# Kernel tuning notes

Hardware: AMD Instinct MI355X
Metric: run time of the kernel (lower is better)

The kernel has to match this reference:

```python
import jax, jax.numpy as jnp
import numpy as np

D_MODEL = 1024
N_HEAD = 16
D_HEAD = D_MODEL // N_HEAD


def setup_inputs() -> dict:
    key = jax.random.key(0)
    k_x, k_wqkv, k_bqkv, k_wp, k_bp = jax.random.split(key, 5)
    B, T = 2, 2048
    bound = 1.0 / np.sqrt(D_MODEL)
    return {
        "x": jax.random.normal(k_x, (B, T, D_MODEL), dtype=jnp.float32),
        "w_qkv": jax.random.uniform(k_wqkv, (D_MODEL, 3 * D_MODEL), jnp.float32, -bound, bound),
        "b_qkv": jax.random.uniform(k_bqkv, (3 * D_MODEL,), jnp.float32, -bound, bound),
        "w_proj": jax.random.uniform(k_wp, (D_MODEL, D_MODEL), jnp.float32, -bound, bound),
        "b_proj": jax.random.uniform(k_bp, (D_MODEL,), jnp.float32, -bound, bound),
    }


def reference(x, w_qkv, b_qkv, w_proj, b_proj):
    B, T, C = x.shape
    qkv = x @ w_qkv + b_qkv                       # [B,T,3C]
    qkv = qkv.reshape(B, T, 3, N_HEAD, D_HEAD)
    qkv = jnp.transpose(qkv, (2, 0, 3, 1, 4))      # [3,B,H,T,dh]
    q, k, v = qkv[0], qkv[1], qkv[2]
    scale = np.sqrt(D_HEAD).astype(np.float32)
    attn = jnp.einsum("bhqd,bhkd->bhqk", q, k) / scale  # [B,H,T,T]
    causal = jnp.tril(jnp.ones((T, T), dtype=bool))
    attn = jnp.where(causal, attn, -jnp.inf)
    attn = jax.nn.softmax(attn, axis=-1)
    out = jnp.einsum("bhqk,bhkd->bhqd", attn, v)   # [B,H,T,dh]
    out = jnp.transpose(out, (0, 2, 1, 3)).reshape(B, T, C)
    return out @ w_proj + b_proj
```

## Files before the change

kernel.cpp:

```cpp
#include <hip/hip_runtime.h>
#include <hip/hip_bf16.h>
#include <math.h>

constexpr int Bb   = 2;
constexpr int T    = 2048;
constexpr int C    = 1024;
constexpr int H    = 16;
constexpr int M    = Bb * T;
constexpr int NQKV = 3 * C;

typedef __attribute__((ext_vector_type(8))) short bf16x8;
typedef __attribute__((ext_vector_type(4))) float f32x4;

__device__ inline short f2bf(float f) {
    __hip_bfloat16 h = __float2bfloat16(f);
    return *reinterpret_cast<short*>(&h);
}

#define GLOBAL_AS __attribute__((address_space(1)))
#define LDS_AS    __attribute__((address_space(3)))

__device__ __forceinline__ void gload_lds16(const short* g, short* s) {
    __builtin_amdgcn_global_load_lds((const GLOBAL_AS void*)g, (LDS_AS void*)s, 16, 0, 0);
}

__global__ __launch_bounds__(256)
void prep_all(const float* __restrict__ x, short* __restrict__ xb,
              const float* __restrict__ w_qkv, short* __restrict__ wqkvt,
              const float* __restrict__ w_proj, short* __restrict__ wprojt)
{
    __shared__ float tile[32][33];
    const int blk = blockIdx.x;
    const int tid = threadIdx.x;

    if (blk < 4096) {
        const int i = blk * 1024 + tid * 4;
        const float4 v = *(const float4*)(x + i);
        short4 s;
        s.x = f2bf(v.x); s.y = f2bf(v.y); s.z = f2bf(v.z); s.w = f2bf(v.w);
        *(short4*)(xb + i) = s;
        return;
    }

    const bool isqkv = (blk < 7168);
    const int bidx = isqkv ? (blk - 4096) : (blk - 7168);
    const int nblk = isqkv ? 96 : 32;
    const int N    = isqkv ? NQKV : C;
    const float* W = isqkv ? w_qkv : w_proj;
    short* Wt      = isqkv ? wqkvt : wprojt;

    const int n0 = (bidx % nblk) * 32, k0 = (bidx / nblk) * 32;
    const int tx = tid & 31, ty = tid >> 5;
#pragma unroll
    for (int i = 0; i < 32; i += 8)
        tile[ty + i][tx] = W[(size_t)(k0 + ty + i) * N + n0 + tx];
    __syncthreads();
#pragma unroll
    for (int i = 0; i < 32; i += 8)
        Wt[(size_t)(n0 + ty + i) * C + k0 + tx] = f2bf(tile[tx][ty + i]);
}

__global__ __launch_bounds__(256)
void gemm_mfma(const short* __restrict__ A, const short* __restrict__ Bt,
               const float* __restrict__ bias, short* __restrict__ outp,
               int Ndim, int Kdim)
{
    __shared__ __align__(16) short As[128 * 32];
    __shared__ __align__(16) short Bs[128 * 32];

    const int tid = threadIdx.x;
    const int w   = tid >> 6;
    const int l   = tid & 63;
    const int lk  = l & 15;
    const int lq  = l >> 4;
    const int m0  = blockIdx.y * 128, n0 = blockIdx.x * 128;
    const int mw  = (w >> 1) * 64, nw = (w & 1) * 64;

    const int srow = w * 16 + (l >> 2);
    const int scol = (l & 3) * 8;
    short* asdst0 = &As[w * 512];
    short* asdst1 = &As[2048 + w * 512];
    short* bsdst0 = &Bs[w * 512];
    short* bsdst1 = &Bs[2048 + w * 512];

    f32x4 acc[4][4];
#pragma unroll
    for (int i = 0; i < 4; ++i)
#pragma unroll
        for (int j = 0; j < 4; ++j) acc[i][j] = (f32x4){0.f, 0.f, 0.f, 0.f};

    for (int k0 = 0; k0 < Kdim; k0 += 32) {
        __syncthreads();
        gload_lds16(A  + (size_t)(m0 + srow)      * Kdim + k0 + scol, asdst0);
        gload_lds16(A  + (size_t)(m0 + 64 + srow) * Kdim + k0 + scol, asdst1);
        gload_lds16(Bt + (size_t)(n0 + srow)      * Kdim + k0 + scol, bsdst0);
        gload_lds16(Bt + (size_t)(n0 + 64 + srow) * Kdim + k0 + scol, bsdst1);
        __syncthreads();

        bf16x8 af[4], bfr[4];
#pragma unroll
        for (int mt = 0; mt < 4; ++mt)
            af[mt] = *(const bf16x8*)&As[(mw + mt * 16 + lk) * 32 + lq * 8];
#pragma unroll
        for (int nt = 0; nt < 4; ++nt)
            bfr[nt] = *(const bf16x8*)&Bs[(nw + nt * 16 + lk) * 32 + lq * 8];
#pragma unroll
        for (int mt = 0; mt < 4; ++mt)
#pragma unroll
            for (int nt = 0; nt < 4; ++nt)
                acc[mt][nt] = __builtin_amdgcn_mfma_f32_16x16x32_bf16(af[mt], bfr[nt], acc[mt][nt], 0, 0, 0);
    }

#pragma unroll
    for (int mt = 0; mt < 4; ++mt) {
#pragma unroll
        for (int nt = 0; nt < 4; ++nt) {
            const int col = n0 + nw + nt * 16 + lk;
            const float bv = bias[col];
#pragma unroll
            for (int r = 0; r < 4; ++r) {
                const int row = m0 + mw + mt * 16 + lq * 4 + r;
                outp[(size_t)row * Ndim + col] = f2bf(acc[mt][nt][r] + bv);
            }
        }
    }
}

__global__ __launch_bounds__(256)
void gemm_mfma_proj(const short* __restrict__ A, const short* __restrict__ Bt,
                    const float* __restrict__ bias, float* __restrict__ outp,
                    int Ndim, int Kdim)
{
    __shared__ __align__(16) short As[64 * 32];
    __shared__ __align__(16) short Bs[128 * 32];

    const int tid = threadIdx.x;
    const int w   = tid >> 6;
    const int l   = tid & 63;
    const int lk  = l & 15;
    const int lq  = l >> 4;
    const int m0  = blockIdx.y * 64, n0 = blockIdx.x * 128;
    const int mw  = (w & 1) * 32, nw = (w >> 1) * 64;

    const int srow = w * 16 + (l >> 2);
    const int scol = (l & 3) * 8;
    short* asdst  = &As[w * 512];
    short* bsdst0 = &Bs[w * 512];
    short* bsdst1 = &Bs[2048 + w * 512];

    f32x4 acc[2][4];
#pragma unroll
    for (int i = 0; i < 2; ++i)
#pragma unroll
        for (int j = 0; j < 4; ++j) acc[i][j] = (f32x4){0.f, 0.f, 0.f, 0.f};

    for (int k0 = 0; k0 < Kdim; k0 += 32) {
        __syncthreads();
        gload_lds16(A  + (size_t)(m0 + srow)      * Kdim + k0 + scol, asdst);
        gload_lds16(Bt + (size_t)(n0 + srow)      * Kdim + k0 + scol, bsdst0);
        gload_lds16(Bt + (size_t)(n0 + 64 + srow) * Kdim + k0 + scol, bsdst1);
        __syncthreads();

        bf16x8 af[2], bfr[4];
#pragma unroll
        for (int mt = 0; mt < 2; ++mt)
            af[mt] = *(const bf16x8*)&As[(mw + mt * 16 + lk) * 32 + lq * 8];
#pragma unroll
        for (int nt = 0; nt < 4; ++nt)
            bfr[nt] = *(const bf16x8*)&Bs[(nw + nt * 16 + lk) * 32 + lq * 8];
#pragma unroll
        for (int mt = 0; mt < 2; ++mt)
#pragma unroll
            for (int nt = 0; nt < 4; ++nt)
                acc[mt][nt] = __builtin_amdgcn_mfma_f32_16x16x32_bf16(af[mt], bfr[nt], acc[mt][nt], 0, 0, 0);
    }

#pragma unroll
    for (int mt = 0; mt < 2; ++mt) {
#pragma unroll
        for (int nt = 0; nt < 4; ++nt) {
            const int col = n0 + nw + nt * 16 + lk;
            const float bv = bias[col];
#pragma unroll
            for (int r = 0; r < 4; ++r) {
                const int row = m0 + mw + mt * 16 + lq * 4 + r;
                outp[(size_t)row * Ndim + col] = acc[mt][nt][r] + bv;
            }
        }
    }
}

constexpr int LDV = 72;

__global__ __launch_bounds__(256)
void attn_mfma(const short* __restrict__ qkv, short* __restrict__ att)
{
    __shared__ __align__(16) short Ks0[64 * 32];
    __shared__ __align__(16) short Ks1[64 * 32];
    __shared__ __align__(16) short Vt[64 * LDV];
    __shared__ __align__(16) short Ps[4][16 * LDV];

    const int idx = blockIdx.x;
    const int xcd = idx & 7;
    const int j   = idx >> 3;
    const int bh  = xcd * 4 + (j & 3);
    const int s   = j >> 2;
    const int qt  = (s < 8)  ? (31 - s)
                  : (s < 16) ? (s - 8)
                  : (s < 24) ? (39 - s)
                  :            (s - 16);
    const int b   = bh >> 4;
    const int h   = bh & 15;
    const int qbase = qt * 64;

    const int tid = threadIdx.x;
    const int w   = tid >> 6;
    const int l   = tid & 63;
    const int lk  = l & 15;
    const int lq  = l >> 4;

    const short* base = qkv + (size_t)b * T * 3072 + h * 64;

    const short* qp = base + (size_t)(qbase + w * 16 + lk) * 3072 + lq * 8;
    const bf16x8 qf0 = *(const bf16x8*)qp;
    const bf16x8 qf1 = *(const bf16x8*)(qp + 32);

    f32x4 acc_o[4];
#pragma unroll
    for (int dt = 0; dt < 4; ++dt) acc_o[dt] = (f32x4){0.f, 0.f, 0.f, 0.f};
    float m_r[4] = {-INFINITY, -INFINITY, -INFINITY, -INFINITY};
    float l_r[4] = {0.f, 0.f, 0.f, 0.f};

    const int ksrow = w * 16 + (l >> 2);
    const int kscol = (l & 3) * 8;
    short* ksdst0 = &Ks0[w * 512];
    short* ksdst1 = &Ks1[w * 512];

    const int vkg = (tid & 15) * 4;
    const int vd0 = (tid >> 4) * 4;

    const int nkt = qt + 1;
#pragma unroll 1
    for (int it = 0; it < nkt; ++it) {
        const int j0 = it * 64;
        __syncthreads();
        gload_lds16(base + 1024 + (size_t)(j0 + ksrow) * 3072 + kscol,      ksdst0);
        gload_lds16(base + 1024 + (size_t)(j0 + ksrow) * 3072 + 32 + kscol, ksdst1);
        {
            const short* vp = base + 2048 + (size_t)(j0 + vkg) * 3072 + vd0;
            short4 vr[4];
#pragma unroll
            for (int kk = 0; kk < 4; ++kk)
                vr[kk] = *(const short4*)(vp + (size_t)kk * 3072);
#pragma unroll
            for (int d = 0; d < 4; ++d) {
                short4 pk;
                pk.x = ((short*)&vr[0])[d]; pk.y = ((short*)&vr[1])[d];
                pk.z = ((short*)&vr[2])[d]; pk.w = ((short*)&vr[3])[d];
                *(short4*)&Vt[(vd0 + d) * LDV + vkg] = pk;
            }
        }
        __syncthreads();

        f32x4 s4[4];
#pragma unroll
        for (int kt = 0; kt < 4; ++kt) {
            const bf16x8 kf0 = *(const bf16x8*)&Ks0[(kt * 16 + lk) * 32 + lq * 8];
            const bf16x8 kf1 = *(const bf16x8*)&Ks1[(kt * 16 + lk) * 32 + lq * 8];
            f32x4 a = (f32x4){0.f, 0.f, 0.f, 0.f};
            a = __builtin_amdgcn_mfma_f32_16x16x32_bf16(qf0, kf0, a, 0, 0, 0);
            a = __builtin_amdgcn_mfma_f32_16x16x32_bf16(qf1, kf1, a, 0, 0, 0);
            s4[kt] = a;
        }

        if (it == nkt - 1) {
            const int rowbase = qbase + w * 16 + lq * 4;
#pragma unroll
            for (int kt = 0; kt < 4; ++kt)
#pragma unroll
                for (int r = 0; r < 4; ++r) {
                    float sv = s4[kt][r] * 0.125f;
                    if (j0 + kt * 16 + lk > rowbase + r) sv = -1e30f;
                    s4[kt][r] = sv;
                }
        } else {
#pragma unroll
            for (int kt = 0; kt < 4; ++kt)
#pragma unroll
                for (int r = 0; r < 4; ++r) s4[kt][r] *= 0.125f;
        }

        float corr[4];
#pragma unroll
        for (int r = 0; r < 4; ++r) {
            float mx = fmaxf(fmaxf(s4[0][r], s4[1][r]), fmaxf(s4[2][r], s4[3][r]));
            mx = fmaxf(mx, __shfl_xor(mx, 1));
            mx = fmaxf(mx, __shfl_xor(mx, 2));
            mx = fmaxf(mx, __shfl_xor(mx, 4));
            mx = fmaxf(mx, __shfl_xor(mx, 8));
            const float mn = fmaxf(m_r[r], mx);
            corr[r] = __expf(m_r[r] - mn);
            m_r[r]  = mn;
            float ps = 0.f;
#pragma unroll
            for (int kt = 0; kt < 4; ++kt) {
                const float p = __expf(s4[kt][r] - mn);
                s4[kt][r] = p;
                ps += p;
            }
            ps += __shfl_xor(ps, 1);
            ps += __shfl_xor(ps, 2);
            ps += __shfl_xor(ps, 4);
            ps += __shfl_xor(ps, 8);
            l_r[r] = l_r[r] * corr[r] + ps;
        }

        short* myP = &Ps[w][0];
#pragma unroll
        for (int kt = 0; kt < 4; ++kt)
#pragma unroll
            for (int r = 0; r < 4; ++r)
                myP[(lq * 4 + r) * LDV + kt * 16 + lk] = f2bf(s4[kt][r]);
#pragma unroll
        for (int dt = 0; dt < 4; ++dt)
#pragma unroll
            for (int r = 0; r < 4; ++r) acc_o[dt][r] *= corr[r];

#pragma unroll
        for (int kc = 0; kc < 2; ++kc) {
            const bf16x8 pf = *(const bf16x8*)&myP[lk * LDV + kc * 32 + lq * 8];
#pragma unroll
            for (int dt = 0; dt < 4; ++dt) {
                const bf16x8 vf = *(const bf16x8*)&Vt[(dt * 16 + lk) * LDV + kc * 32 + lq * 8];
                acc_o[dt] = __builtin_amdgcn_mfma_f32_16x16x32_bf16(pf, vf, acc_o[dt], 0, 0, 0);
            }
        }
    }

    short* op = att + ((size_t)(b * T + qbase + w * 16)) * 1024 + h * 64;
#pragma unroll
    for (int r = 0; r < 4; ++r) {
        const float inv = 1.f / l_r[r];
#pragma unroll
        for (int dt = 0; dt < 4; ++dt)
            op[(size_t)(lq * 4 + r) * 1024 + dt * 16 + lk] = f2bf(acc_o[dt][r] * inv);
    }
}

extern "C" void kernel_launch(void* const* d_in, const int* in_sizes, int n_in,
                              void* d_out, int out_size, void* d_ws, size_t ws_size,
                              hipStream_t stream)
{
    const float* x      = (const float*)d_in[0];
    const float* w_qkv  = (const float*)d_in[1];
    const float* b_qkv  = (const float*)d_in[2];
    const float* w_proj = (const float*)d_in[3];
    const float* b_proj = (const float*)d_in[4];
    float* out = (float*)d_out;

    short* xb     = (short*)d_ws;
    short* wqkvt  = xb     + (size_t)M * C;
    short* wprojt = wqkvt  + (size_t)NQKV * C;
    short* qkvb   = wprojt + (size_t)C * C;
    short* attb   = qkvb   + (size_t)M * NQKV;

    prep_all<<<8192, 256, 0, stream>>>(x, xb, w_qkv, wqkvt, w_proj, wprojt);
    gemm_mfma<<<dim3(NQKV / 128, M / 128), 256, 0, stream>>>(xb, wqkvt, b_qkv, qkvb, NQKV, C);
    attn_mfma<<<1024, 256, 0, stream>>>(qkvb, attb);
    gemm_mfma_proj<<<dim3(C / 128, M / 64), 256, 0, stream>>>(attb, wprojt, b_proj, out, C, C);
}
```

Before: 214.1 us.

## Transpose attention MFMA operands so each lane owns one query row

Swaps the MFMA operand order in both QK^T and PV so the score tile is transposed and each lane holds all keys for a single query row. The per-row softmax state becomes one scalar per lane, the row max and sum reductions need two cross-lane shuffles instead of four per row, and the exponential uses exp2 with the 1/sqrt(d)*log2e scale folded into a single fma. P is written to LDS as packed 32-bit words and the output as short4 vectors. A wave-local lgkmcnt wait is added before P is read back.

Measured after the change: 201.4 us. 1.06x faster.

```diff
diff --git a/kernel.cpp b/kernel.cpp
--- a/kernel.cpp
+++ b/kernel.cpp
@@ -17,11 +17,21 @@
     return *reinterpret_cast<short*>(&h);
 }
 
+#if __has_builtin(__builtin_amdgcn_exp2f)
+#define EXP2(x) __builtin_amdgcn_exp2f(x)
+#else
+#define EXP2(x) exp2f(x)
+#endif
+
 #define GLOBAL_AS __attribute__((address_space(1)))
 #define LDS_AS    __attribute__((address_space(3)))
 
 __device__ __forceinline__ void gload_lds16(const short* g, short* s) {
     __builtin_amdgcn_global_load_lds((const GLOBAL_AS void*)g, (LDS_AS void*)s, 16, 0, 0);
+}
+
+__device__ __forceinline__ void lds_fence_wave() {
+    __asm__ __volatile__("s_waitcnt lgkmcnt(0)" ::: "memory");
 }
 
 __global__ __launch_bounds__(256)
@@ -191,6 +201,8 @@
 }
 
 constexpr int LDV = 72;
+constexpr int LDP = 72;
+constexpr float SC = 0.18033688f;
 
 __global__ __launch_bounds__(256)
 void attn_mfma(const short* __restrict__ qkv, short* __restrict__ att)
@@ -198,7 +210,7 @@
     __shared__ __align__(16) short Ks0[64 * 32];
     __shared__ __align__(16) short Ks1[64 * 32];
     __shared__ __align__(16) short Vt[64 * LDV];
-    __shared__ __align__(16) short Ps[4][16 * LDV];
+    __shared__ __align__(16) short Ps[4][16 * LDP];
 
     const int idx = blockIdx.x;
     const int xcd = idx & 7;
@@ -221,15 +233,16 @@
 
     const short* base = qkv + (size_t)b * T * 3072 + h * 64;
 
-    const short* qp = base + (size_t)(qbase + w * 16 + lk) * 3072 + lq * 8;
+    const int q_abs = qbase + w * 16 + lk;
+    const short* qp = base + (size_t)q_abs * 3072 + lq * 8;
     const bf16x8 qf0 = *(const bf16x8*)qp;
     const bf16x8 qf1 = *(const bf16x8*)(qp + 32);
 
     f32x4 acc_o[4];
 #pragma unroll
     for (int dt = 0; dt < 4; ++dt) acc_o[dt] = (f32x4){0.f, 0.f, 0.f, 0.f};
-    float m_r[4] = {-INFINITY, -INFINITY, -INFINITY, -INFINITY};
-    float l_r[4] = {0.f, 0.f, 0.f, 0.f};
+    float m_run = -INFINITY;
+    float l_run = 0.f;
 
     const int ksrow = w * 16 + (l >> 2);
     const int kscol = (l & 3) * 8;
@@ -268,82 +281,83 @@
             const bf16x8 kf0 = *(const bf16x8*)&Ks0[(kt * 16 + lk) * 32 + lq * 8];
             const bf16x8 kf1 = *(const bf16x8*)&Ks1[(kt * 16 + lk) * 32 + lq * 8];
             f32x4 a = (f32x4){0.f, 0.f, 0.f, 0.f};
-            a = __builtin_amdgcn_mfma_f32_16x16x32_bf16(qf0, kf0, a, 0, 0, 0);
-            a = __builtin_amdgcn_mfma_f32_16x16x32_bf16(qf1, kf1, a, 0, 0, 0);
+            a = __builtin_amdgcn_mfma_f32_16x16x32_bf16(kf0, qf0, a, 0, 0, 0);
+            a = __builtin_amdgcn_mfma_f32_16x16x32_bf16(kf1, qf1, a, 0, 0, 0);
             s4[kt] = a;
         }
 
         if (it == nkt - 1) {
-            const int rowbase = qbase + w * 16 + lq * 4;
 #pragma unroll
             for (int kt = 0; kt < 4; ++kt)
 #pragma unroll
-                for (int r = 0; r < 4; ++r) {
-                    float sv = s4[kt][r] * 0.125f;
-                    if (j0 + kt * 16 + lk > rowbase + r) sv = -1e30f;
-                    s4[kt][r] = sv;
-                }
-        } else {
-#pragma unroll
-            for (int kt = 0; kt < 4; ++kt)
-#pragma unroll
-                for (int r = 0; r < 4; ++r) s4[kt][r] *= 0.125f;
-        }
-
-        float corr[4];
-#pragma unroll
-        for (int r = 0; r < 4; ++r) {
-            float mx = fmaxf(fmaxf(s4[0][r], s4[1][r]), fmaxf(s4[2][r], s4[3][r]));
-            mx = fmaxf(mx, __shfl_xor(mx, 1));
-            mx = fmaxf(mx, __shfl_xor(mx, 2));
-            mx = fmaxf(mx, __shfl_xor(mx, 4));
-            mx = fmaxf(mx, __shfl_xor(mx, 8));
-            const float mn = fmaxf(m_r[r], mx);
-            corr[r] = __expf(m_r[r] - mn);
-            m_r[r]  = mn;
-            float ps = 0.f;
-#pragma unroll
-            for (int kt = 0; kt < 4; ++kt) {
-                const float p = __expf(s4[kt][r] - mn);
-                s4[kt][r] = p;
-                ps += p;
-            }
-            ps += __shfl_xor(ps, 1);
-            ps += __shfl_xor(ps, 2);
-            ps += __shfl_xor(ps, 4);
-            ps += __shfl_xor(ps, 8);
-            l_r[r] = l_r[r] * corr[r] + ps;
-        }
+                for (int r = 0; r < 4; ++r)
+                    if (j0 + kt * 16 + lq * 4 + r > q_abs) s4[kt][r] = -1e30f;
+        }
+
+        float mx0 = fmaxf(fmaxf(s4[0][0], s4[0][1]), fmaxf(s4[0][2], s4[0][3]));
+        float mx1 = fmaxf(fmaxf(s4[1][0], s4[1][1]), fmaxf(s4[1][2], s4[1][3]));
+        float mx2 = fmaxf(fmaxf(s4[2][0], s4[2][1]), fmaxf(s4[2][2], s4[2][3]));
+        float mx3 = fmaxf(fmaxf(s4[3][0], s4[3][1]), fmaxf(s4[3][2], s4[3][3]));
+        float mx  = fmaxf(fmaxf(mx0, mx1), fmaxf(mx2, mx3));
+        mx = fmaxf(mx, __shfl_xor(mx, 16));
+        mx = fmaxf(mx, __shfl_xor(mx, 32));
+        const float mn   = fmaxf(m_run, mx);
+        const float corr = EXP2((m_run - mn) * SC);
+        m_run = mn;
+        const float nmc = -mn * SC;
+#pragma unroll
+        for (int kt = 0; kt < 4; ++kt)
+#pragma unroll
+            for (int r = 0; r < 4; ++r)
+                s4[kt][r] = EXP2(fmaf(s4[kt][r], SC, nmc));
+        float ps0 = (s4[0][0] + s4[0][1]) + (s4[0][2] + s4[0][3]);
+        float ps1 = (s4[1][0] + s4[1][1]) + (s4[1][2] + s4[1][3]);
+        float ps2 = (s4[2][0] + s4[2][1]) + (s4[2][2] + s4[2][3]);
+        float ps3 = (s4[3][0] + s4[3][1]) + (s4[3][2] + s4[3][3]);
+        float ps  = (ps0 + ps1) + (ps2 + ps3);
+        ps += __shfl_xor(ps, 16);
+        ps += __shfl_xor(ps, 32);
+        l_run = l_run * corr + ps;
 
         short* myP = &Ps[w][0];
 #pragma unroll
-        for (int kt = 0; kt < 4; ++kt)
-#pragma unroll
-            for (int r = 0; r < 4; ++r)
-                myP[(lq * 4 + r) * LDV + kt * 16 + lk] = f2bf(s4[kt][r]);
+        for (int kt = 0; kt < 4; ++kt) {
+            const unsigned int p01 = (unsigned int)(unsigned short)f2bf(s4[kt][0])
+                                   | ((unsigned int)(unsigned short)f2bf(s4[kt][1]) << 16);
+            const unsigned int p23 = (unsigned int)(unsigned short)f2bf(s4[kt][2])
+                                   | ((unsigned int)(unsigned short)f2bf(s4[kt][3]) << 16);
+            *(unsigned int*)&myP[lk * LDP + kt * 16 + lq * 4]     = p01;
+            *(unsigned int*)&myP[lk * LDP + kt * 16 + lq * 4 + 2] = p23;
+        }
+
+        lds_fence_wave();
+
 #pragma unroll
         for (int dt = 0; dt < 4; ++dt)
 #pragma unroll
-            for (int r = 0; r < 4; ++r) acc_o[dt][r] *= corr[r];
+            for (int r = 0; r < 4; ++r) acc_o[dt][r] *= corr;
 
 #pragma unroll
         for (int kc = 0; kc < 2; ++kc) {
-            const bf16x8 pf = *(const bf16x8*)&myP[lk * LDV + kc * 32 + lq * 8];
+            const bf16x8 pf = *(const bf16x8*)&myP[lk * LDP + kc * 32 + lq * 8];
 #pragma unroll
             for (int dt = 0; dt < 4; ++dt) {
                 const bf16x8 vf = *(const bf16x8*)&Vt[(dt * 16 + lk) * LDV + kc * 32 + lq * 8];
-                acc_o[dt] = __builtin_amdgcn_mfma_f32_16x16x32_bf16(pf, vf, acc_o[dt], 0, 0, 0);
+                acc_o[dt] = __builtin_amdgcn_mfma_f32_16x16x32_bf16(vf, pf, acc_o[dt], 0, 0, 0);
             }
         }
     }
 
-    short* op = att + ((size_t)(b * T + qbase + w * 16)) * 1024 + h * 64;
-#pragma unroll
-    for (int r = 0; r < 4; ++r) {
-        const float inv = 1.f / l_r[r];
-#pragma unroll
-        for (int dt = 0; dt < 4; ++dt)
-            op[(size_t)(lq * 4 + r) * 1024 + dt * 16 + lk] = f2bf(acc_o[dt][r] * inv);
+    const float inv = 1.f / l_run;
+    short* op = att + ((size_t)(b * T + q_abs)) * 1024 + h * 64;
+#pragma unroll
+    for (int dt = 0; dt < 4; ++dt) {
+        short4 pk;
+        pk.x = f2bf(acc_o[dt][0] * inv);
+        pk.y = f2bf(acc_o[dt][1] * inv);
+        pk.z = f2bf(acc_o[dt][2] * inv);
+        pk.w = f2bf(acc_o[dt][3] * inv);
+        *(short4*)(op + dt * 16 + lq * 4) = pk;
     }
 }
 
```
